# Kernel optimization log

Measured on AMD Instinct MI355X. Metric: run time of the kernel, lower is better.

## Reference

```python
import jax, jax.numpy as jnp
import numpy as np

N, C, P, M = 8, 20, 8732, 16
THRESHOLD, NEG_POS_RATIO, ALPHA = 0.5, 3, 1.0


def cxcy_to_xy(c):
    return jnp.concatenate([c[..., :2] - c[..., 2:] / 2.0, c[..., :2] + c[..., 2:] / 2.0], axis=-1)


def xy_to_cxcy(xy):
    return jnp.concatenate([(xy[..., :2] + xy[..., 2:]) / 2.0, xy[..., 2:] - xy[..., :2]], axis=-1)


def cxcy_to_gcxgcy(cxcy, priors):
    g_cxcy = (cxcy[..., :2] - priors[..., :2]) / (priors[..., 2:] / 10.0)
    g_wh = jnp.log(cxcy[..., 2:] / priors[..., 2:]) * 5.0
    return jnp.concatenate([g_cxcy, g_wh], axis=-1)


def jaccard(a, b):
    # a: (M,4), b: (P,4), boundary coords -> IoU (M,P)
    lo = jnp.maximum(a[:, None, :2], b[None, :, :2])
    hi = jnp.minimum(a[:, None, 2:], b[None, :, 2:])
    inter = jnp.prod(jnp.clip(hi - lo, 0.0), axis=-1)
    area_a = jnp.prod(a[:, 2:] - a[:, :2], axis=-1)
    area_b = jnp.prod(b[:, 2:] - b[:, :2], axis=-1)
    return inter / (area_a[:, None] + area_b[None, :] - inter)


def setup_inputs() -> dict:
    key = jax.random.key(0)
    k1, k2, k3, k4, k5, k6 = jax.random.split(key, 6)
    predicted_locs = jax.random.normal(k1, (N, C, P, 4), jnp.float32)
    predicted_scores = jax.random.normal(k2, (N, C, P, 2), jnp.float32)
    # valid ground-truth boundary boxes (x1<x2, y1<y2) in [0,1]
    ctr = jax.random.uniform(k3, (N, C, M, 2), minval=0.2, maxval=0.8)
    wh = jax.random.uniform(k4, (N, C, M, 2), minval=0.05, maxval=0.3)
    boxes = jnp.concatenate([ctr - wh / 2.0, ctr + wh / 2.0], axis=-1)
    # valid priors in cxcywh (w,h > 0 so log-encoding is finite)
    pctr = jax.random.uniform(k5, (P, 2), minval=0.05, maxval=0.95)
    pwh = jax.random.uniform(k6, (P, 2), minval=0.05, maxval=0.5)
    priors_cxcy = jnp.concatenate([pctr, pwh], axis=-1)
    labels = jnp.ones((N, C, M), jnp.int32)  # binary per-class head: object label = 1
    return {
        "predicted_locs": predicted_locs,
        "predicted_scores": predicted_scores,
        "boxes": boxes,
        "labels": labels,
        "priors_cxcy": priors_cxcy,
    }


def _forward(predicted_locs, predicted_scores, boxes, priors_cxcy, labels):
    n_classes = predicted_scores.shape[1]
    n_priors = predicted_scores.shape[2]
    priors_xy = cxcy_to_xy(priors_cxcy)

    def match(b, lab):
        # b: (M,4) boundary, lab: (M,) int
        ov = jaccard(b, priors_xy)                       # (M,P)
        obj_for_prior = jnp.argmax(ov, axis=0)           # (P,)
        ov_for_prior = jnp.max(ov, axis=0)               # (P,)
        prior_for_obj = jnp.argmax(ov, axis=1)           # (M,)
        # force each object to own its best prior
        obj_for_prior = obj_for_prior.at[prior_for_obj].set(jnp.arange(b.shape[0]))
        ov_for_prior = ov_for_prior.at[prior_for_obj].set(1.0)
        cls = jnp.where(ov_for_prior < THRESHOLD, 0, lab[obj_for_prior])  # (P,)
        tl = cxcy_to_gcxgcy(xy_to_cxcy(b[obj_for_prior]), priors_cxcy)    # (P,4)
        return tl, cls

    true_locs, true_classes = jax.vmap(jax.vmap(match))(boxes, labels)  # (N,C,P,4), (N,C,P)

    pos = true_classes != 0                      # (N,C,P)
    posf = pos.astype(predicted_locs.dtype)
    n_pos_bc = posf.sum(axis=2)                  # (N,C) positives per image per class
    n_pos_c = n_pos_bc.sum(axis=0)               # (C,)

    # localization: mean L1 over positive priors (4 coords each), per class
    l1 = jnp.abs(predicted_locs - true_locs).sum(-1) * posf   # (N,C,P)
    loc_loss_c = l1.sum(axis=(0, 2)) / jnp.maximum(n_pos_c * 4.0, 1.0)

    # per-prior binary cross entropy
    logp = jax.nn.log_softmax(predicted_scores, axis=-1)      # (N,C,P,2)
    ce = -jnp.take_along_axis(logp, true_classes[..., None], axis=-1)[..., 0]  # (N,C,P)
    conf_pos_c = (ce * posf).sum(axis=(0, 2))

    # hard negative mining: sort negatives desc per (image,class) row, keep top 3*n_pos
    ce_neg = jnp.where(pos, 0.0, ce)
    ce_neg_sorted = -jnp.sort(-ce_neg, axis=-1)               # (N,C,P) descending
    n_hard = NEG_POS_RATIO * n_pos_bc                         # (N,C)
    ranks = jnp.arange(n_priors, dtype=n_hard.dtype)
    hard_mask = ranks[None, None, :] < n_hard[..., None]
    conf_hard_c = (ce_neg_sorted * hard_mask).sum(axis=(0, 2))

    safe = jnp.maximum(n_pos_c, 1.0)
    loss_c = jnp.where(
        n_pos_c > 0,
        (conf_pos_c + conf_hard_c + ALPHA * loc_loss_c) / safe,
        0.0,
    ) / n_classes
    return loss_c.sum()


def reference(predicted_locs, predicted_scores, boxes, labels, priors_cxcy):
    return _forward(predicted_locs, predicted_scores, boxes, priors_cxcy, labels)
```

## Files before the change

### kernel.cpp

```cpp
#include <hip/hip_runtime.h>
#include <math.h>

#define NN 8
#define CC 20
#define PP 8732
#define MM 16
#define NPR 3
#define ROWS (NN * CC)

#define SPLIT 12
#define CH 728
#define ABLK 256

#define FBLK 1024
#define EPT 9

__device__ __forceinline__ float fast_rcp(float x) { return __builtin_amdgcn_rcpf(x); }
__device__ __forceinline__ float rfl(float x) {
    return __uint_as_float(__builtin_amdgcn_readfirstlane(__float_as_uint(x)));
}

__device__ __forceinline__ float lse2(float a, float b) {
    float mx = fmaxf(a, b);
    float d  = fabsf(a - b);
    return mx + __logf(1.0f + __expf(-d));
}

__global__ __launch_bounds__(ABLK) void mbox_p1(
    const float* __restrict__ locs, const float* __restrict__ scores,
    const float* __restrict__ boxes, const int* __restrict__ labels,
    const float* __restrict__ priors,
    float* __restrict__ cef, unsigned char* __restrict__ pk8,
    unsigned long long* __restrict__ partials, float* __restrict__ cstats)
{
    const int row = blockIdx.x / SPLIT;
    const int chunk = blockIdx.x - row * SPLIT;
    const int tid = threadIdx.x, lane = tid & 63, wav = tid >> 6;

    __shared__ float s_bcx[MM], s_bcy[MM], s_bw[MM], s_bh[MM];
    __shared__ unsigned int s_pk[4 * MM];
    __shared__ float s_rf[4 * 3];

    float bx1[MM], by1[MM], bx2[MM], by2[MM], bar[MM];
    unsigned int labm = 0;
    {
        const float* bb = boxes + (size_t)row * MM * 4;
        const int*   lb = labels + (size_t)row * MM;
#pragma unroll
        for (int m = 0; m < MM; m++) {
            float x1 = rfl(bb[m * 4 + 0]), y1 = rfl(bb[m * 4 + 1]);
            float x2 = rfl(bb[m * 4 + 2]), y2 = rfl(bb[m * 4 + 3]);
            bx1[m] = x1; by1[m] = y1; bx2[m] = x2; by2[m] = y2;
            bar[m] = rfl((x2 - x1) * (y2 - y1));
            labm |= (lb[m] != 0 ? 1u : 0u) << m;
        }
        labm = __builtin_amdgcn_readfirstlane(labm);
    }
    if (tid < MM) {
        s_bcx[tid] = (bx1[tid] + bx2[tid]) * 0.5f;
        s_bcy[tid] = (by1[tid] + by2[tid]) * 0.5f;
        s_bw[tid]  = bx2[tid] - bx1[tid];
        s_bh[tid]  = by2[tid] - by1[tid];
    }
    __syncthreads();

    const float4* pri4 = (const float4*)priors;
    const float4* loc4 = (const float4*)(locs + (size_t)row * PP * 4);
    const float2* sc2  = (const float2*)(scores + (size_t)row * PP * 2);
    unsigned char* pk  = pk8 + (size_t)row * PP;
    float* cefr        = cef + (size_t)row * PP;

    unsigned int bestk[MM];
#pragma unroll
    for (int m = 0; m < MM; m++) bestk[m] = 0u;
    float l_np = 0.0f, l_l1 = 0.0f, l_cp = 0.0f;
    const int p0 = chunk * CH, p1e = min(p0 + CH, PP);

    float4 pr_next; float2 sc_next;
    if (p0 + tid < p1e) { pr_next = pri4[p0 + tid]; sc_next = sc2[p0 + tid]; }
    int it = 0;
    for (int p = p0 + tid; p < p1e; p += ABLK, ++it) {
        float4 pr = pr_next;
        float2 sc = sc_next;
        if (p + ABLK < p1e) { pr_next = pri4[p + ABLK]; sc_next = sc2[p + ABLK]; }
        const unsigned int lowb = ((unsigned int)(7 - it) << 8) | (unsigned int)(255 - tid);
        float hw = pr.z * 0.5f, hh = pr.w * 0.5f;
        float px1 = pr.x - hw, py1 = pr.y - hh;
        float px2 = pr.x + hw, py2 = pr.y + hh;
        float area_b = (px2 - px1) * (py2 - py1);
        unsigned int bovk = 0u;
#pragma unroll
        for (int m = 0; m < MM; m++) {
            float dx = fminf(bx2[m], px2) - fmaxf(bx1[m], px1);
            float dy = fminf(by2[m], py2) - fmaxf(by1[m], py1);
            dx = fmaxf(dx, 0.0f); dy = fmaxf(dy, 0.0f);
            float inter = dx * dy;
            float den = (bar[m] + area_b) - inter;
            float iou = inter * fast_rcp(den);
            unsigned int ib = __float_as_uint(iou);
            unsigned int km = (ib & 0xFFFFFFF0u) | (unsigned int)(15 - m);
            bovk = max(bovk, km);
            unsigned int kp = (ib & 0xFFFFF800u) | lowb;
            bestk[m] = max(bestk[m], kp);
        }
        int bm = 15 - (int)(bovk & 15u);
        bool pos = (bovk >= 0x3F000000u) && (((labm >> bm) & 1u) != 0u);
        pk[p] = (unsigned char)((pos ? 16u : 0u) | (unsigned)bm);
        float lse = lse2(sc.x, sc.y);
        float ce;
        if (pos) {
            float4 pl = loc4[p];
            l_np += 1.0f;
            l_cp += lse - sc.y;
            float tx = (s_bcx[bm] - pr.x) * 10.0f / pr.z;
            float ty = (s_bcy[bm] - pr.y) * 10.0f / pr.w;
            float tw = __logf(s_bw[bm] / pr.z) * 5.0f;
            float th = __logf(s_bh[bm] / pr.w) * 5.0f;
            l_l1 += fabsf(pl.x - tx) + fabsf(pl.y - ty) + fabsf(pl.z - tw) + fabsf(pl.w - th);
            ce = 0.0f;
        } else {
            ce = fmaxf(lse - sc.x, 0.0f);
        }
        cefr[p] = ce;
    }

#pragma unroll
    for (int m = 0; m < MM; m++) {
        unsigned int key = bestk[m];
#pragma unroll
        for (int off = 32; off; off >>= 1) {
            unsigned int o = __shfl_down(key, off);
            if (o > key) key = o;
        }
        if (lane == 0) s_pk[wav * MM + m] = key;
    }
#pragma unroll
    for (int off = 32; off; off >>= 1) {
        l_np += __shfl_down(l_np, off);
        l_l1 += __shfl_down(l_l1, off);
        l_cp += __shfl_down(l_cp, off);
    }
    if (lane == 0) { s_rf[wav * 3] = l_np; s_rf[wav * 3 + 1] = l_l1; s_rf[wav * 3 + 2] = l_cp; }
    __syncthreads();
    if (tid < MM) {
        unsigned int key = s_pk[tid];
        for (int w = 1; w < 4; w++) {
            unsigned int o = s_pk[w * MM + tid];
            if (o > key) key = o;
        }
        int tw  = 255 - (int)(key & 255u);
        int itw = 7 - (int)((key >> 8) & 7u);
        int pm  = p0 + itw * ABLK + tw;
        partials[((size_t)row * MM + tid) * SPLIT + chunk] =
            ((unsigned long long)(key & 0xFFFFF800u) << 32) |
            (unsigned int)(0x7fffffff - pm);
    }
    if (tid == 0) {
        float np = 0, l1 = 0, cp = 0;
        for (int w = 0; w < 4; w++) { np += s_rf[w * 3]; l1 += s_rf[w * 3 + 1]; cp += s_rf[w * 3 + 2]; }
        float* cs = cstats + ((size_t)row * SPLIT + chunk) * 3;
        cs[0] = np; cs[1] = l1; cs[2] = cp;
    }
}

__global__ __launch_bounds__(FBLK) void mbox_sel(
    const float* __restrict__ locs, const float* __restrict__ scores,
    const float* __restrict__ boxes, const int* __restrict__ labels,
    const float* __restrict__ priors,
    const float* __restrict__ cef, const unsigned char* __restrict__ pk8,
    const unsigned long long* __restrict__ partials,
    const float* __restrict__ cstats, float* __restrict__ rstats)
{
    const int row = blockIdx.x, tid = threadIdx.x, lane = tid & 63, wav = tid >> 6;

    __shared__ unsigned int s_u32[PP];
    __shared__ float s_bcx[MM], s_bcy[MM], s_bw[MM], s_bh[MM];
    __shared__ int s_lab[MM], s_pfo[MM];
    __shared__ float s_sum[3];
    __shared__ unsigned int s_hist[256];
    __shared__ unsigned int s_prefix, s_Kr, s_K;
    __shared__ float s_redf[16];
    __shared__ int s_redi[16];

    if (tid < MM) {
        const float* b = boxes + ((size_t)row * MM + tid) * 4;
        float x1 = b[0], y1 = b[1], x2 = b[2], y2 = b[3];
        s_bcx[tid] = (x1 + x2) * 0.5f; s_bcy[tid] = (y1 + y2) * 0.5f;
        s_bw[tid] = x2 - x1; s_bh[tid] = y2 - y1;
        s_lab[tid] = labels[row * MM + tid];
        const unsigned long long* pr = partials + ((size_t)row * MM + tid) * SPLIT;
        unsigned long long key = pr[0];
        for (int c = 1; c < SPLIT; c++) { unsigned long long o = pr[c]; if (o > key) key = o; }
        s_pfo[tid] = 0x7fffffff - (int)(unsigned)(key & 0xffffffffull);
    }
    if (tid >= 16 && tid < 19) {
        int j = tid - 16; float s = 0;
        for (int c = 0; c < SPLIT; c++) s += cstats[((size_t)row * SPLIT + c) * 3 + j];
        s_sum[j] = s;
    }
#pragma unroll
    for (int k = 0; k < EPT; k++) {
        const int p = tid + k * FBLK;
        if (p < PP) s_u32[p] = __float_as_uint(cef[(size_t)row * PP + p]);
    }
    __syncthreads();

    const float4* loc4 = (const float4*)(locs + (size_t)row * PP * 4);
    const float2* sc2  = (const float2*)(scores + (size_t)row * PP * 2);
    float d_np = 0, d_l1 = 0, d_cp = 0;
    if (tid < MM) {
        int p = s_pfo[tid];
        bool is_last = true;
        for (int mm = tid + 1; mm < MM; mm++) if (s_pfo[mm] == p) is_last = false;
        if (is_last) {
            const float4 pr = ((const float4*)priors)[p];
            const float4 pl = loc4[p];
            const float2 sc = sc2[p];
            float lse = lse2(sc.x, sc.y);
            unsigned int u = pk8[(size_t)row * PP + p];
            if (u & 16u) {
                int mo = u & 15;
                d_np -= 1.0f; d_cp -= (lse - sc.y);
                float tx = (s_bcx[mo] - pr.x) * 10.0f / pr.z;
                float ty = (s_bcy[mo] - pr.y) * 10.0f / pr.w;
                float tw = __logf(s_bw[mo] / pr.z) * 5.0f;
                float th = __logf(s_bh[mo] / pr.w) * 5.0f;
                d_l1 -= fabsf(pl.x - tx) + fabsf(pl.y - ty) + fabsf(pl.z - tw) + fabsf(pl.w - th);
            }
            if (s_lab[tid] != 0) {
                d_np += 1.0f; d_cp += (lse - sc.y);
                float tx = (s_bcx[tid] - pr.x) * 10.0f / pr.z;
                float ty = (s_bcy[tid] - pr.y) * 10.0f / pr.w;
                float tw = __logf(s_bw[tid] / pr.z) * 5.0f;
                float th = __logf(s_bh[tid] / pr.w) * 5.0f;
                d_l1 += fabsf(pl.x - tx) + fabsf(pl.y - ty) + fabsf(pl.z - tw) + fabsf(pl.w - th);
                s_u32[p] = 0u;
            } else {
                s_u32[p] = __float_as_uint(fmaxf(lse - sc.x, 0.0f));
            }
        }
    }
    if (tid < 64) {
#pragma unroll
        for (int off = 32; off; off >>= 1) {
            d_np += __shfl_down(d_np, off);
            d_l1 += __shfl_down(d_l1, off);
            d_cp += __shfl_down(d_cp, off);
        }
        if (tid == 0) {
            float np = s_sum[0] + d_np;
            rstats[(size_t)row * 8 + 0] = np;
            rstats[(size_t)row * 8 + 1] = s_sum[1] + d_l1;
            rstats[(size_t)row * 8 + 2] = s_sum[2] + d_cp;
            int K = NPR * (int)(np + 0.5f);
            s_K = (K > 0) ? (unsigned)K : 0u;
            s_prefix = 0u;
            s_Kr = (K > 0) ? (unsigned)K : 0u;
        }
    }
    __syncthreads();

    const unsigned int K = s_K;
    unsigned int T = 0u;
    if (K > 0u && K < PP) {
        for (int pass = 0; pass < 4; pass++) {
            const int shift = 24 - 8 * pass;
            if (tid < 256) s_hist[tid] = 0u;
            __syncthreads();
            const unsigned int pref   = s_prefix;
            const unsigned int maskhi = (pass == 0) ? 0u : (0xffffffffu << (shift + 8));
#pragma unroll
            for (int k = 0; k < EPT; k++) {
                const int p = tid + k * FBLK;
                unsigned int u = (p < PP) ? s_u32[p] : 0u;
                if ((u & maskhi) == pref) atomicAdd(&s_hist[(u >> shift) & 255u], 1u);
            }
            __syncthreads();
            if (wav == 0) {
                unsigned int Kr = s_Kr;
                unsigned int h0 = s_hist[lane * 4 + 0];
                unsigned int h1 = s_hist[lane * 4 + 1];
                unsigned int h2 = s_hist[lane * 4 + 2];
                unsigned int h3 = s_hist[lane * 4 + 3];
                unsigned int c3 = h3;
                unsigned int c2 = h3 + h2;
                unsigned int c1 = c2 + h1;
                unsigned int c0 = c1 + h0;
                unsigned int suf = c0;
#pragma unroll
                for (int off = 1; off < 64; off <<= 1) {
                    unsigned int o = __shfl_down(suf, off);
                    if (lane + off < 64) suf += o;
                }
                unsigned int above = suf - c0;
                int cand = -1;
                unsigned int G = 0;
                if      (c3 + above >= Kr) { cand = lane * 4 + 3; G = above + c3 - h3; }
                else if (c2 + above >= Kr) { cand = lane * 4 + 2; G = above + c2 - h2; }
                else if (c1 + above >= Kr) { cand = lane * 4 + 1; G = above + c1 - h1; }
                else if (c0 + above >= Kr) { cand = lane * 4 + 0; G = above + c0 - h0; }
                int best = cand;
#pragma unroll
                for (int off = 32; off; off >>= 1) best = max(best, __shfl_down(best, off));
                best = __shfl(best, 0);
                if (cand == best && cand >= 0) {
                    s_Kr = Kr - G;
                    s_prefix = pref | ((unsigned int)best << shift);
                }
            }
            __syncthreads();
        }
        T = s_prefix;
    }

    float sgt = 0.0f; int cgt = 0;
    if (K > 0u) {
#pragma unroll
        for (int k = 0; k < EPT; k++) {
            const int p = tid + k * FBLK;
            unsigned int u = (p < PP) ? s_u32[p] : 0u;
            if (u > T) { sgt += __uint_as_float(u); cgt++; }
        }
    }
#pragma unroll
    for (int off = 32; off; off >>= 1) {
        sgt += __shfl_down(sgt, off);
        cgt += __shfl_down(cgt, off);
    }
    if (lane == 0) { s_redf[wav] = sgt; s_redi[wav] = cgt; }
    __syncthreads();
    if (tid == 0) {
        float s = 0; int cnt = 0;
        for (int w = 0; w < 16; w++) { s += s_redf[w]; cnt += s_redi[w]; }
        float chard = (K > 0u) ? (s + (float)(int)(K - (unsigned)cnt) * __uint_as_float(T)) : 0.0f;
        rstats[(size_t)row * 8 + 4] = chard;
    }
}

__global__ void mbox_finalize(const float* __restrict__ rstats, float* __restrict__ out) {
    int c = threadIdx.x;
    float loss = 0.0f;
    if (c < CC) {
        float np = 0, l1 = 0, cp = 0, ch = 0;
        for (int n = 0; n < NN; n++) {
            const float* s = rstats + ((size_t)(n * CC + c)) * 8;
            np += s[0]; l1 += s[1]; cp += s[2]; ch += s[4];
        }
        float loc = l1 / fmaxf(np * 4.0f, 1.0f);
        float val = (np > 0.0f) ? (cp + ch + loc) / fmaxf(np, 1.0f) : 0.0f;
        loss = val / (float)CC;
    }
#pragma unroll
    for (int off = 32; off; off >>= 1) loss += __shfl_down(loss, off);
    if (threadIdx.x == 0) out[0] = loss;
}

extern "C" void kernel_launch(void* const* d_in, const int* in_sizes, int n_in,
                              void* d_out, int out_size, void* d_ws, size_t ws_size,
                              hipStream_t stream) {
    const float* locs   = (const float*)d_in[0];
    const float* scores = (const float*)d_in[1];
    const float* boxes  = (const float*)d_in[2];
    const int*   labels = (const int*)d_in[3];
    const float* priors = (const float*)d_in[4];
    float* out = (float*)d_out;

    char* ws = (char*)d_ws;
    float* cef                   = (float*)ws;
    unsigned char* pk8           = (unsigned char*)(ws + 5588480);
    unsigned long long* partials = (unsigned long long*)(ws + 6985600);
    float* cstats                = (float*)(ws + 7231360);
    float* rstats                = (float*)(ws + 7254400);

    mbox_p1<<<ROWS * SPLIT, ABLK, 0, stream>>>(locs, scores, boxes, labels, priors,
                                               cef, pk8, partials, cstats);
    mbox_sel<<<ROWS, FBLK, 0, stream>>>(locs, scores, boxes, labels, priors,
                                        cef, pk8, partials, cstats, rstats);
    mbox_finalize<<<1, 64, 0, stream>>>(rstats, out);
}
```

Baseline: 121.6 us.

## Fuse match, selection and finalize into one kernel via last-block atomics

Merges the three kernels into a single launch. Each row's last-finishing chunk block, found with an atomic counter, runs the radix-select hard-negative mining directly from global cef memory with 256 threads. The globally last block then computes the final loss. This removes two kernel launches and the separate 1024-thread selection pass, but adds a memset, threadfences, and a selection tail that now runs with fewer threads and reads global memory instead of LDS.

```diff
diff --git a/kernel.cpp b/kernel.cpp
--- a/kernel.cpp
+++ b/kernel.cpp
@@ -7,13 +7,16 @@
 #define MM 16
 #define NPR 3
 #define ROWS (NN * CC)
-
 #define SPLIT 12
 #define CH 728
 #define ABLK 256
-
-#define FBLK 1024
-#define EPT 9
+#define EPS 35
+
+#define OFF_PK8   5588480
+#define OFF_PART  6985600
+#define OFF_CST   7231360
+#define OFF_RST   7254400
+#define OFF_CNT   7259520
 
 __device__ __forceinline__ float fast_rcp(float x) { return __builtin_amdgcn_rcpf(x); }
 __device__ __forceinline__ float rfl(float x) {
@@ -26,12 +29,14 @@
     return mx + __logf(1.0f + __expf(-d));
 }
 
-__global__ __launch_bounds__(ABLK) void mbox_p1(
+__global__ __launch_bounds__(ABLK) void mbox_one(
     const float* __restrict__ locs, const float* __restrict__ scores,
     const float* __restrict__ boxes, const int* __restrict__ labels,
     const float* __restrict__ priors,
     float* __restrict__ cef, unsigned char* __restrict__ pk8,
-    unsigned long long* __restrict__ partials, float* __restrict__ cstats)
+    unsigned long long* __restrict__ partials, float* __restrict__ cstats,
+    float* __restrict__ rstats, int* __restrict__ rowcnt,
+    int* __restrict__ donecnt, float* __restrict__ out)
 {
     const int row = blockIdx.x / SPLIT;
     const int chunk = blockIdx.x - row * SPLIT;
@@ -40,6 +45,13 @@
     __shared__ float s_bcx[MM], s_bcy[MM], s_bw[MM], s_bh[MM];
     __shared__ unsigned int s_pk[4 * MM];
     __shared__ float s_rf[4 * 3];
+    __shared__ int s_flag;
+    __shared__ int s_pfo[MM];
+    __shared__ float s_sum[3];
+    __shared__ unsigned int s_hist[256];
+    __shared__ unsigned int s_prefix, s_Kr, s_K;
+    __shared__ float s_redf[4];
+    __shared__ int s_redi[4];
 
     float bx1[MM], by1[MM], bx2[MM], by2[MM], bar[MM];
     unsigned int labm = 0;
@@ -98,10 +110,8 @@
             float den = (bar[m] + area_b) - inter;
             float iou = inter * fast_rcp(den);
             unsigned int ib = __float_as_uint(iou);
-            unsigned int km = (ib & 0xFFFFFFF0u) | (unsigned int)(15 - m);
-            bovk = max(bovk, km);
-            unsigned int kp = (ib & 0xFFFFF800u) | lowb;
-            bestk[m] = max(bestk[m], kp);
+            bovk = max(bovk, (ib & 0xFFFFFFF0u) | (unsigned int)(15 - m));
+            bestk[m] = max(bestk[m], (ib & 0xFFFFF800u) | lowb);
         }
         int bm = 15 - (int)(bovk & 15u);
         bool pos = (bovk >= 0x3F000000u) && (((labm >> bm) & 1u) != 0u);
@@ -161,33 +171,17 @@
         float* cs = cstats + ((size_t)row * SPLIT + chunk) * 3;
         cs[0] = np; cs[1] = l1; cs[2] = cp;
     }
-}
-
-__global__ __launch_bounds__(FBLK) void mbox_sel(
-    const float* __restrict__ locs, const float* __restrict__ scores,
-    const float* __restrict__ boxes, const int* __restrict__ labels,
-    const float* __restrict__ priors,
-    const float* __restrict__ cef, const unsigned char* __restrict__ pk8,
-    const unsigned long long* __restrict__ partials,
-    const float* __restrict__ cstats, float* __restrict__ rstats)
-{
-    const int row = blockIdx.x, tid = threadIdx.x, lane = tid & 63, wav = tid >> 6;
-
-    __shared__ unsigned int s_u32[PP];
-    __shared__ float s_bcx[MM], s_bcy[MM], s_bw[MM], s_bh[MM];
-    __shared__ int s_lab[MM], s_pfo[MM];
-    __shared__ float s_sum[3];
-    __shared__ unsigned int s_hist[256];
-    __shared__ unsigned int s_prefix, s_Kr, s_K;
-    __shared__ float s_redf[16];
-    __shared__ int s_redi[16];
+    __syncthreads();
+
+    if (tid == 0) {
+        __threadfence();
+        s_flag = (atomicAdd(&rowcnt[row], 1) == SPLIT - 1) ? 1 : 0;
+    }
+    __syncthreads();
+    if (!s_flag) return;
+    __threadfence();
 
     if (tid < MM) {
-        const float* b = boxes + ((size_t)row * MM + tid) * 4;
-        float x1 = b[0], y1 = b[1], x2 = b[2], y2 = b[3];
-        s_bcx[tid] = (x1 + x2) * 0.5f; s_bcy[tid] = (y1 + y2) * 0.5f;
-        s_bw[tid] = x2 - x1; s_bh[tid] = y2 - y1;
-        s_lab[tid] = labels[row * MM + tid];
         const unsigned long long* pr = partials + ((size_t)row * MM + tid) * SPLIT;
         unsigned long long key = pr[0];
         for (int c = 1; c < SPLIT; c++) { unsigned long long o = pr[c]; if (o > key) key = o; }
@@ -198,26 +192,19 @@
         for (int c = 0; c < SPLIT; c++) s += cstats[((size_t)row * SPLIT + c) * 3 + j];
         s_sum[j] = s;
     }
-#pragma unroll
-    for (int k = 0; k < EPT; k++) {
-        const int p = tid + k * FBLK;
-        if (p < PP) s_u32[p] = __float_as_uint(cef[(size_t)row * PP + p]);
-    }
-    __syncthreads();
-
-    const float4* loc4 = (const float4*)(locs + (size_t)row * PP * 4);
-    const float2* sc2  = (const float2*)(scores + (size_t)row * PP * 2);
+    __syncthreads();
+
     float d_np = 0, d_l1 = 0, d_cp = 0;
     if (tid < MM) {
         int p = s_pfo[tid];
         bool is_last = true;
         for (int mm = tid + 1; mm < MM; mm++) if (s_pfo[mm] == p) is_last = false;
         if (is_last) {
-            const float4 pr = ((const float4*)priors)[p];
+            const float4 pr = pri4[p];
             const float4 pl = loc4[p];
             const float2 sc = sc2[p];
             float lse = lse2(sc.x, sc.y);
-            unsigned int u = pk8[(size_t)row * PP + p];
+            unsigned int u = pk[p];
             if (u & 16u) {
                 int mo = u & 15;
                 d_np -= 1.0f; d_cp -= (lse - sc.y);
@@ -227,17 +214,19 @@
                 float th = __logf(s_bh[mo] / pr.w) * 5.0f;
                 d_l1 -= fabsf(pl.x - tx) + fabsf(pl.y - ty) + fabsf(pl.z - tw) + fabsf(pl.w - th);
             }
-            if (s_lab[tid] != 0) {
+            float nce;
+            if ((labm >> tid) & 1u) {
                 d_np += 1.0f; d_cp += (lse - sc.y);
                 float tx = (s_bcx[tid] - pr.x) * 10.0f / pr.z;
                 float ty = (s_bcy[tid] - pr.y) * 10.0f / pr.w;
                 float tw = __logf(s_bw[tid] / pr.z) * 5.0f;
                 float th = __logf(s_bh[tid] / pr.w) * 5.0f;
                 d_l1 += fabsf(pl.x - tx) + fabsf(pl.y - ty) + fabsf(pl.z - tw) + fabsf(pl.w - th);
-                s_u32[p] = 0u;
+                nce = 0.0f;
             } else {
-                s_u32[p] = __float_as_uint(fmaxf(lse - sc.x, 0.0f));
-            }
+                nce = fmaxf(lse - sc.x, 0.0f);
+            }
+            cefr[p] = nce;
         }
     }
     if (tid < 64) {
@@ -265,15 +254,16 @@
     if (K > 0u && K < PP) {
         for (int pass = 0; pass < 4; pass++) {
             const int shift = 24 - 8 * pass;
-            if (tid < 256) s_hist[tid] = 0u;
+            s_hist[tid & 255] = 0u;
             __syncthreads();
             const unsigned int pref   = s_prefix;
             const unsigned int maskhi = (pass == 0) ? 0u : (0xffffffffu << (shift + 8));
-#pragma unroll
-            for (int k = 0; k < EPT; k++) {
-                const int p = tid + k * FBLK;
-                unsigned int u = (p < PP) ? s_u32[p] : 0u;
-                if ((u & maskhi) == pref) atomicAdd(&s_hist[(u >> shift) & 255u], 1u);
+            for (int k = 0; k < EPS; k++) {
+                const int p = tid + (k << 8);
+                if (p < PP) {
+                    unsigned int u = __float_as_uint(cefr[p]);
+                    if ((u & maskhi) == pref) atomicAdd(&s_hist[(u >> shift) & 255u], 1u);
+                }
             }
             __syncthreads();
             if (wav == 0) {
@@ -315,11 +305,12 @@
 
     float sgt = 0.0f; int cgt = 0;
     if (K > 0u) {
-#pragma unroll
-        for (int k = 0; k < EPT; k++) {
-            const int p = tid + k * FBLK;
-            unsigned int u = (p < PP) ? s_u32[p] : 0u;
-            if (u > T) { sgt += __uint_as_float(u); cgt++; }
+        for (int k = 0; k < EPS; k++) {
+            const int p = tid + (k << 8);
+            if (p < PP) {
+                unsigned int u = __float_as_uint(cefr[p]);
+                if (u > T) { sgt += __uint_as_float(u); cgt++; }
+            }
         }
     }
 #pragma unroll
@@ -331,28 +322,33 @@
     __syncthreads();
     if (tid == 0) {
         float s = 0; int cnt = 0;
-        for (int w = 0; w < 16; w++) { s += s_redf[w]; cnt += s_redi[w]; }
+        for (int w = 0; w < 4; w++) { s += s_redf[w]; cnt += s_redi[w]; }
         float chard = (K > 0u) ? (s + (float)(int)(K - (unsigned)cnt) * __uint_as_float(T)) : 0.0f;
         rstats[(size_t)row * 8 + 4] = chard;
-    }
-}
-
-__global__ void mbox_finalize(const float* __restrict__ rstats, float* __restrict__ out) {
-    int c = threadIdx.x;
-    float loss = 0.0f;
-    if (c < CC) {
-        float np = 0, l1 = 0, cp = 0, ch = 0;
-        for (int n = 0; n < NN; n++) {
-            const float* s = rstats + ((size_t)(n * CC + c)) * 8;
-            np += s[0]; l1 += s[1]; cp += s[2]; ch += s[4];
-        }
-        float loc = l1 / fmaxf(np * 4.0f, 1.0f);
-        float val = (np > 0.0f) ? (cp + ch + loc) / fmaxf(np, 1.0f) : 0.0f;
-        loss = val / (float)CC;
-    }
-#pragma unroll
-    for (int off = 32; off; off >>= 1) loss += __shfl_down(loss, off);
-    if (threadIdx.x == 0) out[0] = loss;
+        __threadfence();
+        s_flag = (atomicAdd(donecnt, 1) == ROWS - 1) ? 1 : 0;
+    }
+    __syncthreads();
+    if (!s_flag) return;
+    __threadfence();
+
+    if (tid < 64) {
+        int c = tid;
+        float loss = 0.0f;
+        if (c < CC) {
+            float np = 0, l1 = 0, cp = 0, ch = 0;
+            for (int n = 0; n < NN; n++) {
+                const float* s = rstats + ((size_t)(n * CC + c)) * 8;
+                np += s[0]; l1 += s[1]; cp += s[2]; ch += s[4];
+            }
+            float loc = l1 / fmaxf(np * 4.0f, 1.0f);
+            float val = (np > 0.0f) ? (cp + ch + loc) / fmaxf(np, 1.0f) : 0.0f;
+            loss = val / (float)CC;
+        }
+#pragma unroll
+        for (int off = 32; off; off >>= 1) loss += __shfl_down(loss, off);
+        if (tid == 0) out[0] = loss;
+    }
 }
 
 extern "C" void kernel_launch(void* const* d_in, const int* in_sizes, int n_in,
@@ -367,14 +363,15 @@
 
     char* ws = (char*)d_ws;
     float* cef                   = (float*)ws;
-    unsigned char* pk8           = (unsigned char*)(ws + 5588480);
-    unsigned long long* partials = (unsigned long long*)(ws + 6985600);
-    float* cstats                = (float*)(ws + 7231360);
-    float* rstats                = (float*)(ws + 7254400);
-
-    mbox_p1<<<ROWS * SPLIT, ABLK, 0, stream>>>(locs, scores, boxes, labels, priors,
-                                               cef, pk8, partials, cstats);
-    mbox_sel<<<ROWS, FBLK, 0, stream>>>(locs, scores, boxes, labels, priors,
-                                        cef, pk8, partials, cstats, rstats);
-    mbox_finalize<<<1, 64, 0, stream>>>(rstats, out);
+    unsigned char* pk8           = (unsigned char*)(ws + OFF_PK8);
+    unsigned long long* partials = (unsigned long long*)(ws + OFF_PART);
+    float* cstats                = (float*)(ws + OFF_CST);
+    float* rstats                = (float*)(ws + OFF_RST);
+    int* rowcnt                  = (int*)(ws + OFF_CNT);
+    int* donecnt                 = (int*)(ws + OFF_CNT + ROWS * 4);
+
+    hipMemsetAsync(ws + OFF_CNT, 0, ROWS * 4 + 4, stream);
+    mbox_one<<<ROWS * SPLIT, ABLK, 0, stream>>>(locs, scores, boxes, labels, priors,
+                                                cef, pk8, partials, cstats, rstats,
+                                                rowcnt, donecnt, out);
 }
```

Measured after the change: 257.6 us. +111.8%, slower.

## Drop per-prior match byte buffer and fuse finalize into selection kernel

Applied to the files above, without the earlier changes.

Stops writing the per-prior packed match byte array in the first pass. The selection kernel now recomputes the best-box match for the few forced-match priors it needs. The separate finalize launch is removed: the last block of the selection kernel, found through an atomic done-counter that the first kernel resets, reduces the per-row stats and writes the loss. This trades a small amount of recompute and atomics for one fewer launch and less global write traffic.

```diff
diff --git a/kernel.cpp b/kernel.cpp
--- a/kernel.cpp
+++ b/kernel.cpp
@@ -7,13 +7,16 @@
 #define MM 16
 #define NPR 3
 #define ROWS (NN * CC)
-
 #define SPLIT 12
 #define CH 728
 #define ABLK 256
-
 #define FBLK 1024
 #define EPT 9
+
+#define OFF_PART  5588480
+#define OFF_CST   5834240
+#define OFF_RST   5857280
+#define OFF_CNT   5862400
 
 __device__ __forceinline__ float fast_rcp(float x) { return __builtin_amdgcn_rcpf(x); }
 __device__ __forceinline__ float rfl(float x) {
@@ -30,12 +33,15 @@
     const float* __restrict__ locs, const float* __restrict__ scores,
     const float* __restrict__ boxes, const int* __restrict__ labels,
     const float* __restrict__ priors,
-    float* __restrict__ cef, unsigned char* __restrict__ pk8,
-    unsigned long long* __restrict__ partials, float* __restrict__ cstats)
+    float* __restrict__ cef,
+    unsigned long long* __restrict__ partials, float* __restrict__ cstats,
+    int* __restrict__ donecnt)
 {
     const int row = blockIdx.x / SPLIT;
     const int chunk = blockIdx.x - row * SPLIT;
     const int tid = threadIdx.x, lane = tid & 63, wav = tid >> 6;
+
+    if (blockIdx.x == 0 && tid == 0) *donecnt = 0;
 
     __shared__ float s_bcx[MM], s_bcy[MM], s_bw[MM], s_bh[MM];
     __shared__ unsigned int s_pk[4 * MM];
@@ -67,7 +73,6 @@
     const float4* pri4 = (const float4*)priors;
     const float4* loc4 = (const float4*)(locs + (size_t)row * PP * 4);
     const float2* sc2  = (const float2*)(scores + (size_t)row * PP * 2);
-    unsigned char* pk  = pk8 + (size_t)row * PP;
     float* cefr        = cef + (size_t)row * PP;
 
     unsigned int bestk[MM];
@@ -98,14 +103,11 @@
             float den = (bar[m] + area_b) - inter;
             float iou = inter * fast_rcp(den);
             unsigned int ib = __float_as_uint(iou);
-            unsigned int km = (ib & 0xFFFFFFF0u) | (unsigned int)(15 - m);
-            bovk = max(bovk, km);
-            unsigned int kp = (ib & 0xFFFFF800u) | lowb;
-            bestk[m] = max(bestk[m], kp);
+            bovk = max(bovk, (ib & 0xFFFFFFF0u) | (unsigned int)(15 - m));
+            bestk[m] = max(bestk[m], (ib & 0xFFFFF800u) | lowb);
         }
         int bm = 15 - (int)(bovk & 15u);
         bool pos = (bovk >= 0x3F000000u) && (((labm >> bm) & 1u) != 0u);
-        pk[p] = (unsigned char)((pos ? 16u : 0u) | (unsigned)bm);
         float lse = lse2(sc.x, sc.y);
         float ce;
         if (pos) {
@@ -167,13 +169,15 @@
     const float* __restrict__ locs, const float* __restrict__ scores,
     const float* __restrict__ boxes, const int* __restrict__ labels,
     const float* __restrict__ priors,
-    const float* __restrict__ cef, const unsigned char* __restrict__ pk8,
+    const float* __restrict__ cef,
     const unsigned long long* __restrict__ partials,
-    const float* __restrict__ cstats, float* __restrict__ rstats)
+    const float* __restrict__ cstats, float* __restrict__ rstats,
+    int* __restrict__ donecnt, float* __restrict__ out)
 {
     const int row = blockIdx.x, tid = threadIdx.x, lane = tid & 63, wav = tid >> 6;
 
     __shared__ unsigned int s_u32[PP];
+    __shared__ float s_bx1[MM], s_by1[MM], s_bx2[MM], s_by2[MM], s_bar[MM];
     __shared__ float s_bcx[MM], s_bcy[MM], s_bw[MM], s_bh[MM];
     __shared__ int s_lab[MM], s_pfo[MM];
     __shared__ float s_sum[3];
@@ -181,10 +185,13 @@
     __shared__ unsigned int s_prefix, s_Kr, s_K;
     __shared__ float s_redf[16];
     __shared__ int s_redi[16];
+    __shared__ int s_flag;
 
     if (tid < MM) {
         const float* b = boxes + ((size_t)row * MM + tid) * 4;
         float x1 = b[0], y1 = b[1], x2 = b[2], y2 = b[3];
+        s_bx1[tid] = x1; s_by1[tid] = y1; s_bx2[tid] = x2; s_by2[tid] = y2;
+        s_bar[tid] = (x2 - x1) * (y2 - y1);
         s_bcx[tid] = (x1 + x2) * 0.5f; s_bcy[tid] = (y1 + y2) * 0.5f;
         s_bw[tid] = x2 - x1; s_bh[tid] = y2 - y1;
         s_lab[tid] = labels[row * MM + tid];
@@ -205,6 +212,7 @@
     }
     __syncthreads();
 
+    const float4* pri4 = (const float4*)priors;
     const float4* loc4 = (const float4*)(locs + (size_t)row * PP * 4);
     const float2* sc2  = (const float2*)(scores + (size_t)row * PP * 2);
     float d_np = 0, d_l1 = 0, d_cp = 0;
@@ -213,13 +221,28 @@
         bool is_last = true;
         for (int mm = tid + 1; mm < MM; mm++) if (s_pfo[mm] == p) is_last = false;
         if (is_last) {
-            const float4 pr = ((const float4*)priors)[p];
+            const float4 pr = pri4[p];
             const float4 pl = loc4[p];
             const float2 sc = sc2[p];
             float lse = lse2(sc.x, sc.y);
-            unsigned int u = pk8[(size_t)row * PP + p];
-            if (u & 16u) {
-                int mo = u & 15;
+            float hw = pr.z * 0.5f, hh = pr.w * 0.5f;
+            float px1 = pr.x - hw, py1 = pr.y - hh;
+            float px2 = pr.x + hw, py2 = pr.y + hh;
+            float area_b = (px2 - px1) * (py2 - py1);
+            unsigned int bovk = 0u;
+            for (int m = 0; m < MM; m++) {
+                float dx = fminf(s_bx2[m], px2) - fmaxf(s_bx1[m], px1);
+                float dy = fminf(s_by2[m], py2) - fmaxf(s_by1[m], py1);
+                dx = fmaxf(dx, 0.0f); dy = fmaxf(dy, 0.0f);
+                float inter = dx * dy;
+                float den = (s_bar[m] + area_b) - inter;
+                float iou = inter * fast_rcp(den);
+                unsigned int ib = __float_as_uint(iou);
+                bovk = max(bovk, (ib & 0xFFFFFFF0u) | (unsigned int)(15 - m));
+            }
+            int mo = 15 - (int)(bovk & 15u);
+            bool waspos = (bovk >= 0x3F000000u) && (s_lab[mo] != 0);
+            if (waspos) {
                 d_np -= 1.0f; d_cp -= (lse - sc.y);
                 float tx = (s_bcx[mo] - pr.x) * 10.0f / pr.z;
                 float ty = (s_bcy[mo] - pr.y) * 10.0f / pr.w;
@@ -249,9 +272,12 @@
         }
         if (tid == 0) {
             float np = s_sum[0] + d_np;
-            rstats[(size_t)row * 8 + 0] = np;
-            rstats[(size_t)row * 8 + 1] = s_sum[1] + d_l1;
-            rstats[(size_t)row * 8 + 2] = s_sum[2] + d_cp;
+            __hip_atomic_store(&rstats[(size_t)row * 8 + 0], np,
+                               __ATOMIC_RELAXED, __HIP_MEMORY_SCOPE_AGENT);
+            __hip_atomic_store(&rstats[(size_t)row * 8 + 1], s_sum[1] + d_l1,
+                               __ATOMIC_RELAXED, __HIP_MEMORY_SCOPE_AGENT);
+            __hip_atomic_store(&rstats[(size_t)row * 8 + 2], s_sum[2] + d_cp,
+                               __ATOMIC_RELAXED, __HIP_MEMORY_SCOPE_AGENT);
             int K = NPR * (int)(np + 0.5f);
             s_K = (K > 0) ? (unsigned)K : 0u;
             s_prefix = 0u;
@@ -333,26 +359,35 @@
         float s = 0; int cnt = 0;
         for (int w = 0; w < 16; w++) { s += s_redf[w]; cnt += s_redi[w]; }
         float chard = (K > 0u) ? (s + (float)(int)(K - (unsigned)cnt) * __uint_as_float(T)) : 0.0f;
-        rstats[(size_t)row * 8 + 4] = chard;
-    }
-}
-
-__global__ void mbox_finalize(const float* __restrict__ rstats, float* __restrict__ out) {
-    int c = threadIdx.x;
-    float loss = 0.0f;
-    if (c < CC) {
-        float np = 0, l1 = 0, cp = 0, ch = 0;
-        for (int n = 0; n < NN; n++) {
-            const float* s = rstats + ((size_t)(n * CC + c)) * 8;
-            np += s[0]; l1 += s[1]; cp += s[2]; ch += s[4];
-        }
-        float loc = l1 / fmaxf(np * 4.0f, 1.0f);
-        float val = (np > 0.0f) ? (cp + ch + loc) / fmaxf(np, 1.0f) : 0.0f;
-        loss = val / (float)CC;
-    }
-#pragma unroll
-    for (int off = 32; off; off >>= 1) loss += __shfl_down(loss, off);
-    if (threadIdx.x == 0) out[0] = loss;
+        __hip_atomic_store(&rstats[(size_t)row * 8 + 4], chard,
+                           __ATOMIC_RELAXED, __HIP_MEMORY_SCOPE_AGENT);
+        int old = __hip_atomic_fetch_add(donecnt, 1, __ATOMIC_ACQ_REL,
+                                         __HIP_MEMORY_SCOPE_AGENT);
+        s_flag = (old == ROWS - 1) ? 1 : 0;
+    }
+    __syncthreads();
+    if (!s_flag) return;
+
+    if (tid < 64) {
+        int c = tid;
+        float loss = 0.0f;
+        if (c < CC) {
+            float np = 0, l1 = 0, cp = 0, ch = 0;
+            for (int n = 0; n < NN; n++) {
+                const float* s = rstats + ((size_t)(n * CC + c)) * 8;
+                np += __hip_atomic_load(&s[0], __ATOMIC_ACQUIRE, __HIP_MEMORY_SCOPE_AGENT);
+                l1 += __hip_atomic_load(&s[1], __ATOMIC_ACQUIRE, __HIP_MEMORY_SCOPE_AGENT);
+                cp += __hip_atomic_load(&s[2], __ATOMIC_ACQUIRE, __HIP_MEMORY_SCOPE_AGENT);
+                ch += __hip_atomic_load(&s[4], __ATOMIC_ACQUIRE, __HIP_MEMORY_SCOPE_AGENT);
+            }
+            float loc = l1 / fmaxf(np * 4.0f, 1.0f);
+            float val = (np > 0.0f) ? (cp + ch + loc) / fmaxf(np, 1.0f) : 0.0f;
+            loss = val / (float)CC;
+        }
+#pragma unroll
+        for (int off = 32; off; off >>= 1) loss += __shfl_down(loss, off);
+        if (tid == 0) out[0] = loss;
+    }
 }
 
 extern "C" void kernel_launch(void* const* d_in, const int* in_sizes, int n_in,
@@ -367,14 +402,13 @@
 
     char* ws = (char*)d_ws;
     float* cef                   = (float*)ws;
-    unsigned char* pk8           = (unsigned char*)(ws + 5588480);
-    unsigned long long* partials = (unsigned long long*)(ws + 6985600);
-    float* cstats                = (float*)(ws + 7231360);
-    float* rstats                = (float*)(ws + 7254400);
+    unsigned long long* partials = (unsigned long long*)(ws + OFF_PART);
+    float* cstats                = (float*)(ws + OFF_CST);
+    float* rstats                = (float*)(ws + OFF_RST);
+    int* donecnt                 = (int*)(ws + OFF_CNT);
 
     mbox_p1<<<ROWS * SPLIT, ABLK, 0, stream>>>(locs, scores, boxes, labels, priors,
-                                               cef, pk8, partials, cstats);
+                                               cef, partials, cstats, donecnt);
     mbox_sel<<<ROWS, FBLK, 0, stream>>>(locs, scores, boxes, labels, priors,
-                                        cef, pk8, partials, cstats, rstats);
-    mbox_finalize<<<1, 64, 0, stream>>>(rstats, out);
+                                        cef, partials, cstats, rstats, donecnt, out);
 }
```

New measurement: 128.7 us. 1.06x slower.
